# Performance work log

Measured on AMD Instinct MI355X. Metric: run time of the kernel, lower is better.

The kernel has to match this reference:

```python
import jax, jax.numpy as jnp
import numpy as np

N, E, G = 20000, 320000, 64
IN, HID, HEADS, EDGE_D, ACT = 128, 256, 4, 5, 8
NEG_SLOPE = 0.2


def setup_inputs() -> dict:
    key = jax.random.key(0)
    ks = jax.random.split(key, 24)
    g = lambda i, shape, scale=0.05: jax.random.normal(ks[i], shape, dtype=jnp.float32) * scale
    inp = {
        "x": jax.random.normal(ks[0], (N, IN), dtype=jnp.float32),
        "edge_index": jax.random.randint(ks[1], (2, E), 0, N, dtype=jnp.int64),
        "batch": jnp.sort(jax.random.randint(ks[2], (N,), 0, G, dtype=jnp.int64)),
        "edge_attr": jax.random.normal(ks[3], (E, EDGE_D), dtype=jnp.float32),
        # GATv2 layer 1: in->64 per head, 4 heads, concat -> 256
        "W1l": g(4, (IN, HID)), "W1r": g(5, (IN, HID)), "W1e": g(6, (EDGE_D, HID)),
        "att1": g(7, (HEADS, HID // HEADS)), "b1": jnp.zeros((HID,), jnp.float32),
        # GATv2 layer 2: 256->256, 1 head
        "W2l": g(8, (HID, HID)), "W2r": g(9, (HID, HID)), "W2e": g(10, (EDGE_D, HID)),
        "att2": g(11, (1, HID)), "b2": jnp.zeros((HID,), jnp.float32),
        # heads
        "Wp": g(12, (HID, ACT)), "bp": jnp.zeros((ACT,), jnp.float32),
        "Wv": g(13, (HID, 1)), "bv": jnp.zeros((1,), jnp.float32),
    }
    return inp


def gatv2_conv(x, src, dst, edge_attr, Wl, Wr, We, att, bias, heads, concat):
    # PyG GATv2Conv (share_weights=False, add_self_loops=False):
    #   x_l = lin_l(x) (source msg), x_r = lin_r(x) (target), e = lin_edge(edge_attr)
    #   score = att . leaky_relu(x_l[src] + x_r[dst] + e); segment-softmax over dst
    #   out[i] = sum_j alpha_ij * x_l[j]
    n = x.shape[0]
    c = Wl.shape[1] // heads
    xl = (x @ Wl).reshape(n, heads, c)
    xr = (x @ Wr).reshape(n, heads, c)
    e = (edge_attr @ We).reshape(-1, heads, c)
    m = jax.nn.leaky_relu(xl[src] + xr[dst] + e, NEG_SLOPE)      # [E, H, C]
    logit = jnp.einsum("ehc,hc->eh", m, att)                      # [E, H]
    lmax = jax.ops.segment_max(logit, dst, num_segments=n)        # [N, H]
    unnorm = jnp.exp(logit - lmax[dst])
    denom = jax.ops.segment_sum(unnorm, dst, num_segments=n)
    alpha = unnorm / (denom[dst] + 1e-16)                         # [E, H]
    out = jax.ops.segment_sum(alpha[:, :, None] * xl[src], dst, num_segments=n)  # [N,H,C]
    out = out.reshape(n, heads * c) if concat else out.mean(axis=1)
    return out + bias


def reference(x, edge_index, batch, edge_attr,
              W1l, W1r, W1e, att1, b1,
              W2l, W2r, W2e, att2, b2,
              Wp, bp, Wv, bv):
    src, dst = edge_index[0], edge_index[1]
    h = gatv2_conv(x, src, dst, edge_attr, W1l, W1r, W1e, att1, b1, HEADS, True)
    h = jax.nn.relu(h)  # dropout p=0.0 -> identity
    h = gatv2_conv(h, src, dst, edge_attr, W2l, W2r, W2e, att2, b2, 1, False)
    h = jax.nn.relu(h)
    # global mean pool over graphs
    sums = jax.ops.segment_sum(h, batch, num_segments=G)
    cnt = jax.ops.segment_sum(jnp.ones((h.shape[0],), h.dtype), batch, num_segments=G)
    g = sums / jnp.maximum(cnt, 1.0)[:, None]
    logits = g @ Wp + bp                 # [G, ACT]
    value = (g @ Wv + bv)[:, 0]          # [G]
    # deterministic outputs (sampling excluded): concat logits and value
    return jnp.concatenate([logits, value[:, None]], axis=-1)  # [G, ACT+1]
```

## Files before the change

### kernel.cpp

```cpp
#include <hip/hip_runtime.h>
#include <math.h>

#define NN 20000
#define NE 320000
#define NG 64
#define IND 128
#define HIDD 256
#define NH 4
#define ED 5
#define NACT 8
#define NEG 0.2f
#define MAXDEG 64

__global__ __launch_bounds__(256) void gemm64(const float* __restrict__ A,
    const float* __restrict__ B, float* __restrict__ C, int M, int K, int Ncol)
{
    const int BK = 32;
    __shared__ float As[32][68];
    __shared__ float Bs[32][64];
    int bm = blockIdx.x * 64, bn = blockIdx.y * 64;
    int tid = threadIdx.x;
    int tx = tid & 15, ty = tid >> 4;
    float acc[4][4] = {};
    for (int k0 = 0; k0 < K; k0 += BK) {
        for (int idx = tid; idx < 64 * BK; idx += 256) {
            int r = idx >> 5, c = idx & 31;
            int gr = bm + r;
            As[c][r] = (gr < M) ? A[(size_t)gr * K + k0 + c] : 0.f;
        }
        for (int idx = tid; idx < BK * 64; idx += 256) {
            int r = idx >> 6, c = idx & 63;
            Bs[r][c] = B[(size_t)(k0 + r) * Ncol + bn + c];
        }
        __syncthreads();
        #pragma unroll
        for (int k = 0; k < BK; ++k) {
            float4 a4 = *(const float4*)&As[k][ty * 4];
            float4 b4 = *(const float4*)&Bs[k][tx * 4];
            float a[4] = {a4.x, a4.y, a4.z, a4.w};
            float b[4] = {b4.x, b4.y, b4.z, b4.w};
            #pragma unroll
            for (int i = 0; i < 4; ++i)
                #pragma unroll
                for (int j = 0; j < 4; ++j)
                    acc[i][j] = fmaf(a[i], b[j], acc[i][j]);
        }
        __syncthreads();
    }
    #pragma unroll
    for (int i = 0; i < 4; ++i) {
        int r = bm + ty * 4 + i;
        if (r < M) {
            float4 v = {acc[i][0], acc[i][1], acc[i][2], acc[i][3]};
            *(float4*)&C[(size_t)r * Ncol + bn + tx * 4] = v;
        }
    }
}

__global__ __launch_bounds__(256) void build_slots(const int* __restrict__ dst,
    int* __restrict__ deg, int* __restrict__ slots)
{
    int e = blockIdx.x * 256 + threadIdx.x;
    if (e >= NE) return;
    int d = dst[e];
    int pos = atomicAdd(&deg[d], 1);
    if (pos < MAXDEG) slots[d * MAXDEG + pos] = e;
}

template <int HEADS_T>
__global__ __launch_bounds__(256) void fused_agg(
    const int* __restrict__ deg, const int* __restrict__ slots,
    const int* __restrict__ src, const float* __restrict__ eattr,
    const float* __restrict__ xl, const float* __restrict__ xr,
    const float* __restrict__ We, const float* __restrict__ attw,
    const float* __restrict__ bias, float* __restrict__ out)
{
    __shared__ float sWe[ED * HIDD];
    __shared__ float sAtt[HIDD];
    for (int i = threadIdx.x; i < ED * HIDD; i += 256) sWe[i] = We[i];
    for (int i = threadIdx.x; i < HIDD; i += 256) sAtt[i] = attw[i];
    __syncthreads();

    int wave = threadIdx.x >> 6, lane = threadIdx.x & 63;
    int n = blockIdx.x * 4 + wave;
    int dg = min(deg[n], MAXDEG);
    int c0 = lane * 4;

    float attr_[4], wer[ED][4];
    #pragma unroll
    for (int j = 0; j < 4; ++j) attr_[j] = sAtt[c0 + j];
    #pragma unroll
    for (int k = 0; k < ED; ++k)
        #pragma unroll
        for (int j = 0; j < 4; ++j) wer[k][j] = sWe[k * HIDD + c0 + j];

    float4 xr4 = *(const float4*)(xr + (size_t)n * HIDD + c0);
    float xra[4] = {xr4.x, xr4.y, xr4.z, xr4.w};

    float denom = 0.f;
    float acc[4] = {0.f, 0.f, 0.f, 0.f};

    const int* slotrow = slots + (size_t)n * MAXDEG;
    for (int i = 0; i < dg; ++i) {
        int e = slotrow[i];
        int s = src[e];
        float4 xl4 = *(const float4*)(xl + (size_t)s * HIDD + c0);
        float xla[4] = {xl4.x, xl4.y, xl4.z, xl4.w};
        float ea[ED];
        #pragma unroll
        for (int k = 0; k < ED; ++k) ea[k] = eattr[(size_t)e * ED + k];
        float partial = 0.f;
        #pragma unroll
        for (int j = 0; j < 4; ++j) {
            float ev = 0.f;
            #pragma unroll
            for (int k = 0; k < ED; ++k) ev = fmaf(ea[k], wer[k][j], ev);
            float m = xla[j] + xra[j] + ev;
            m = m > 0.f ? m : NEG * m;
            partial = fmaf(m, attr_[j], partial);
        }
        if (HEADS_T == 4) {
            #pragma unroll
            for (int off = 1; off < 16; off <<= 1)
                partial += __shfl_xor(partial, off, 64);
        } else {
            #pragma unroll
            for (int off = 1; off < 64; off <<= 1)
                partial += __shfl_xor(partial, off, 64);
        }
        float ex = expf(partial);
        denom += ex;
        #pragma unroll
        for (int j = 0; j < 4; ++j) acc[j] = fmaf(ex, xla[j], acc[j]);
    }
    float inv = 1.f / (denom + 1e-16f);
    float4 o;
    o.x = fmaxf(acc[0] * inv + bias[c0 + 0], 0.f);
    o.y = fmaxf(acc[1] * inv + bias[c0 + 1], 0.f);
    o.z = fmaxf(acc[2] * inv + bias[c0 + 2], 0.f);
    o.w = fmaxf(acc[3] * inv + bias[c0 + 3], 0.f);
    *(float4*)(out + (size_t)n * HIDD + c0) = o;
}

#define POOL_CHUNK 128
__global__ __launch_bounds__(256) void pool_kernel(
    const float* __restrict__ h, const int* __restrict__ batch,
    float* __restrict__ pool, float* __restrict__ cnt)
{
    int c = threadIdx.x;
    int start = blockIdx.x * POOL_CHUNK;
    int end = min(start + POOL_CHUNK, NN);
    if (start >= NN) return;
    float acc = 0.f;
    int cur = batch[start];
    int localCount = 0;
    for (int n = start; n < end; ++n) {
        int g = batch[n];
        if (g != cur) {
            atomicAdd(&pool[cur * HIDD + c], acc);
            if (c == 0) atomicAdd(&cnt[cur], (float)localCount);
            acc = 0.f; localCount = 0; cur = g;
        }
        acc += h[(size_t)n * HIDD + c];
        ++localCount;
    }
    atomicAdd(&pool[cur * HIDD + c], acc);
    if (c == 0) atomicAdd(&cnt[cur], (float)localCount);
}

__global__ __launch_bounds__(256) void head_kernel(
    const float* __restrict__ pool, const float* __restrict__ cnt,
    const float* __restrict__ Wp, const float* __restrict__ bp,
    const float* __restrict__ Wv, const float* __restrict__ bv,
    float* __restrict__ out)
{
    int g = blockIdx.x;
    int c = threadIdx.x;
    float gv = pool[g * HIDD + c] / fmaxf(cnt[g], 1.0f);
    __shared__ float red[256];
    for (int j = 0; j < NACT + 1; ++j) {
        float w = (j < NACT) ? Wp[c * NACT + j] : Wv[c];
        red[c] = gv * w;
        __syncthreads();
        for (int sl = 128; sl > 0; sl >>= 1) {
            if (c < sl) red[c] += red[c + sl];
            __syncthreads();
        }
        if (c == 0) out[g * (NACT + 1) + j] = red[0] + ((j < NACT) ? bp[j] : bv[0]);
        __syncthreads();
    }
}

extern "C" void kernel_launch(void* const* d_in, const int* in_sizes, int n_in,
                              void* d_out, int out_size, void* d_ws, size_t ws_size,
                              hipStream_t stream)
{
    const float* x    = (const float*)d_in[0];
    const int*   ei   = (const int*)d_in[1];
    const int*   batch= (const int*)d_in[2];
    const float* ea   = (const float*)d_in[3];
    const float* W1l  = (const float*)d_in[4];
    const float* W1r  = (const float*)d_in[5];
    const float* W1e  = (const float*)d_in[6];
    const float* att1 = (const float*)d_in[7];
    const float* b1   = (const float*)d_in[8];
    const float* W2l  = (const float*)d_in[9];
    const float* W2r  = (const float*)d_in[10];
    const float* W2e  = (const float*)d_in[11];
    const float* att2 = (const float*)d_in[12];
    const float* b2   = (const float*)d_in[13];
    const float* Wp   = (const float*)d_in[14];
    const float* bp   = (const float*)d_in[15];
    const float* Wv   = (const float*)d_in[16];
    const float* bv   = (const float*)d_in[17];
    const int* src = ei;
    const int* dst = ei + NE;
    float* out = (float*)d_out;

    float* ws = (float*)d_ws;
    size_t off = 0;
    float* A     = ws + off; off += (size_t)NN * HIDD;
    float* B     = ws + off; off += (size_t)NN * HIDD;
    float* C     = ws + off; off += (size_t)NN * HIDD;
    float* D     = ws + off; off += (size_t)NN * HIDD;
    float* pool  = ws + off; off += (size_t)NG * HIDD;
    float* cnt   = ws + off; off += NG;
    int*   deg   = (int*)(ws + off); off += NN;
    int*   slots = (int*)(ws + off); off += (size_t)NN * MAXDEG;

    hipMemsetAsync(pool, 0, (size_t)(NG * HIDD + NG + NN) * sizeof(float), stream);

    build_slots<<<(NE + 255) / 256, 256, 0, stream>>>(dst, deg, slots);

    dim3 ggrid((NN + 63) / 64, HIDD / 64);
    gemm64<<<ggrid, 256, 0, stream>>>(x, W1l, A, NN, IND, HIDD);
    gemm64<<<ggrid, 256, 0, stream>>>(x, W1r, B, NN, IND, HIDD);
    fused_agg<4><<<NN / 4, 256, 0, stream>>>(deg, slots, src, ea, A, B, W1e, att1, b1, C);

    gemm64<<<ggrid, 256, 0, stream>>>(C, W2l, A, NN, HIDD, HIDD);
    gemm64<<<ggrid, 256, 0, stream>>>(C, W2r, B, NN, HIDD, HIDD);
    fused_agg<1><<<NN / 4, 256, 0, stream>>>(deg, slots, src, ea, A, B, W2e, att2, b2, D);

    pool_kernel<<<(NN + POOL_CHUNK - 1) / POOL_CHUNK, 256, 0, stream>>>(D, batch, pool, cnt);
    head_kernel<<<NG, 256, 0, stream>>>(pool, cnt, Wp, bp, Wv, bv, out);
}
```

Before: 485.0 us.

## Enlarge GEMM tiles, batch l/r GEMMs, and prefetch edge data per lane in aggregation

The GEMM now uses 128x64 tiles with 8x4 outputs per thread and handles both left and right weight matrices in one launch via blockIdx.z, halving the launches and raising reuse per thread. The aggregation kernel preloads each neighbour's slot, source index and edge attributes into one lane each, then broadcasts them with shuffles instead of reloading them serially. It also processes two edges per iteration so their gathers and reductions overlap. Register pressure goes up in both kernels, and the As padding of 129 may cause LDS bank conflicts or misaligned float4 reads.

```diff
diff --git a/kernel.cpp b/kernel.cpp
--- a/kernel.cpp
+++ b/kernel.cpp
@@ -12,35 +12,43 @@
 #define NEG 0.2f
 #define MAXDEG 64
 
-__global__ __launch_bounds__(256) void gemm64(const float* __restrict__ A,
-    const float* __restrict__ B, float* __restrict__ C, int M, int K, int Ncol)
-{
-    const int BK = 32;
-    __shared__ float As[32][68];
+__global__ __launch_bounds__(256) void gemm128x64(
+    const float* __restrict__ A, const float* __restrict__ Bl,
+    const float* __restrict__ Br, float* __restrict__ Cl, float* __restrict__ Cr,
+    int M, int K, int Ncol)
+{
+    const float* B = blockIdx.z ? Br : Bl;
+    float*       C = blockIdx.z ? Cr : Cl;
+    __shared__ float As[32][129];
     __shared__ float Bs[32][64];
-    int bm = blockIdx.x * 64, bn = blockIdx.y * 64;
+    int bm = blockIdx.x * 128, bn = blockIdx.y * 64;
     int tid = threadIdx.x;
     int tx = tid & 15, ty = tid >> 4;
-    float acc[4][4] = {};
-    for (int k0 = 0; k0 < K; k0 += BK) {
-        for (int idx = tid; idx < 64 * BK; idx += 256) {
+    float acc[8][4] = {};
+    for (int k0 = 0; k0 < K; k0 += 32) {
+        #pragma unroll
+        for (int t = 0; t < 16; ++t) {
+            int idx = tid + t * 256;
             int r = idx >> 5, c = idx & 31;
             int gr = bm + r;
             As[c][r] = (gr < M) ? A[(size_t)gr * K + k0 + c] : 0.f;
         }
-        for (int idx = tid; idx < BK * 64; idx += 256) {
+        #pragma unroll
+        for (int t = 0; t < 8; ++t) {
+            int idx = tid + t * 256;
             int r = idx >> 6, c = idx & 63;
             Bs[r][c] = B[(size_t)(k0 + r) * Ncol + bn + c];
         }
         __syncthreads();
         #pragma unroll
-        for (int k = 0; k < BK; ++k) {
-            float4 a4 = *(const float4*)&As[k][ty * 4];
-            float4 b4 = *(const float4*)&Bs[k][tx * 4];
-            float a[4] = {a4.x, a4.y, a4.z, a4.w};
-            float b[4] = {b4.x, b4.y, b4.z, b4.w};
-            #pragma unroll
-            for (int i = 0; i < 4; ++i)
+        for (int k = 0; k < 32; ++k) {
+            float4 a0 = *(const float4*)&As[k][ty * 8];
+            float4 a1 = *(const float4*)&As[k][ty * 8 + 4];
+            float4 b0 = *(const float4*)&Bs[k][tx * 4];
+            float a[8] = {a0.x, a0.y, a0.z, a0.w, a1.x, a1.y, a1.z, a1.w};
+            float b[4] = {b0.x, b0.y, b0.z, b0.w};
+            #pragma unroll
+            for (int i = 0; i < 8; ++i)
                 #pragma unroll
                 for (int j = 0; j < 4; ++j)
                     acc[i][j] = fmaf(a[i], b[j], acc[i][j]);
@@ -48,8 +56,8 @@
         __syncthreads();
     }
     #pragma unroll
-    for (int i = 0; i < 4; ++i) {
-        int r = bm + ty * 4 + i;
+    for (int i = 0; i < 8; ++i) {
+        int r = bm + ty * 8 + i;
         if (r < M) {
             float4 v = {acc[i][0], acc[i][1], acc[i][2], acc[i][3]};
             *(float4*)&C[(size_t)r * Ncol + bn + tx * 4] = v;
@@ -97,42 +105,100 @@
     float4 xr4 = *(const float4*)(xr + (size_t)n * HIDD + c0);
     float xra[4] = {xr4.x, xr4.y, xr4.z, xr4.w};
 
+    int s_l = 0;
+    float ea_l[ED] = {0.f, 0.f, 0.f, 0.f, 0.f};
+    if (lane < dg) {
+        int e_l = slots[(size_t)n * MAXDEG + lane];
+        s_l = src[e_l];
+        #pragma unroll
+        for (int k = 0; k < ED; ++k) ea_l[k] = eattr[(size_t)e_l * ED + k];
+    }
+
     float denom = 0.f;
     float acc[4] = {0.f, 0.f, 0.f, 0.f};
 
-    const int* slotrow = slots + (size_t)n * MAXDEG;
-    for (int i = 0; i < dg; ++i) {
-        int e = slotrow[i];
-        int s = src[e];
-        float4 xl4 = *(const float4*)(xl + (size_t)s * HIDD + c0);
-        float xla[4] = {xl4.x, xl4.y, xl4.z, xl4.w};
-        float ea[ED];
-        #pragma unroll
-        for (int k = 0; k < ED; ++k) ea[k] = eattr[(size_t)e * ED + k];
-        float partial = 0.f;
+    int i = 0;
+    for (; i + 2 <= dg; i += 2) {
+        int sA = __shfl(s_l, i, 64);
+        int sB = __shfl(s_l, i + 1, 64);
+        float eaA[ED], eaB[ED];
+        #pragma unroll
+        for (int k = 0; k < ED; ++k) {
+            eaA[k] = __shfl(ea_l[k], i, 64);
+            eaB[k] = __shfl(ea_l[k], i + 1, 64);
+        }
+        float4 xA4 = *(const float4*)(xl + (size_t)sA * HIDD + c0);
+        float4 xB4 = *(const float4*)(xl + (size_t)sB * HIDD + c0);
+        float xlA[4] = {xA4.x, xA4.y, xA4.z, xA4.w};
+        float xlB[4] = {xB4.x, xB4.y, xB4.z, xB4.w};
+        float pA = 0.f, pB = 0.f;
         #pragma unroll
         for (int j = 0; j < 4; ++j) {
-            float ev = 0.f;
-            #pragma unroll
-            for (int k = 0; k < ED; ++k) ev = fmaf(ea[k], wer[k][j], ev);
-            float m = xla[j] + xra[j] + ev;
-            m = m > 0.f ? m : NEG * m;
-            partial = fmaf(m, attr_[j], partial);
+            float evA = 0.f, evB = 0.f;
+            #pragma unroll
+            for (int k = 0; k < ED; ++k) {
+                evA = fmaf(eaA[k], wer[k][j], evA);
+                evB = fmaf(eaB[k], wer[k][j], evB);
+            }
+            float mA = xlA[j] + xra[j] + evA;
+            float mB = xlB[j] + xra[j] + evB;
+            mA = mA > 0.f ? mA : NEG * mA;
+            mB = mB > 0.f ? mB : NEG * mB;
+            pA = fmaf(mA, attr_[j], pA);
+            pB = fmaf(mB, attr_[j], pB);
         }
         if (HEADS_T == 4) {
             #pragma unroll
-            for (int off = 1; off < 16; off <<= 1)
-                partial += __shfl_xor(partial, off, 64);
+            for (int off = 1; off < 16; off <<= 1) {
+                pA += __shfl_xor(pA, off, 64);
+                pB += __shfl_xor(pB, off, 64);
+            }
         } else {
             #pragma unroll
-            for (int off = 1; off < 64; off <<= 1)
-                partial += __shfl_xor(partial, off, 64);
-        }
-        float ex = expf(partial);
-        denom += ex;
-        #pragma unroll
-        for (int j = 0; j < 4; ++j) acc[j] = fmaf(ex, xla[j], acc[j]);
-    }
+            for (int off = 1; off < 64; off <<= 1) {
+                pA += __shfl_xor(pA, off, 64);
+                pB += __shfl_xor(pB, off, 64);
+            }
+        }
+        float exA = expf(pA);
+        float exB = expf(pB);
+        denom += exA;
+        denom += exB;
+        #pragma unroll
+        for (int j = 0; j < 4; ++j) acc[j] = fmaf(exA, xlA[j], acc[j]);
+        #pragma unroll
+        for (int j = 0; j < 4; ++j) acc[j] = fmaf(exB, xlB[j], acc[j]);
+    }
+    if (i < dg) {
+        int sA = __shfl(s_l, i, 64);
+        float eaA[ED];
+        #pragma unroll
+        for (int k = 0; k < ED; ++k) eaA[k] = __shfl(ea_l[k], i, 64);
+        float4 xA4 = *(const float4*)(xl + (size_t)sA * HIDD + c0);
+        float xlA[4] = {xA4.x, xA4.y, xA4.z, xA4.w};
+        float pA = 0.f;
+        #pragma unroll
+        for (int j = 0; j < 4; ++j) {
+            float evA = 0.f;
+            #pragma unroll
+            for (int k = 0; k < ED; ++k) evA = fmaf(eaA[k], wer[k][j], evA);
+            float mA = xlA[j] + xra[j] + evA;
+            mA = mA > 0.f ? mA : NEG * mA;
+            pA = fmaf(mA, attr_[j], pA);
+        }
+        if (HEADS_T == 4) {
+            #pragma unroll
+            for (int off = 1; off < 16; off <<= 1) pA += __shfl_xor(pA, off, 64);
+        } else {
+            #pragma unroll
+            for (int off = 1; off < 64; off <<= 1) pA += __shfl_xor(pA, off, 64);
+        }
+        float exA = expf(pA);
+        denom += exA;
+        #pragma unroll
+        for (int j = 0; j < 4; ++j) acc[j] = fmaf(exA, xlA[j], acc[j]);
+    }
+
     float inv = 1.f / (denom + 1e-16f);
     float4 o;
     o.x = fmaxf(acc[0] * inv + bias[c0 + 0], 0.f);
@@ -232,13 +298,11 @@
 
     build_slots<<<(NE + 255) / 256, 256, 0, stream>>>(dst, deg, slots);
 
-    dim3 ggrid((NN + 63) / 64, HIDD / 64);
-    gemm64<<<ggrid, 256, 0, stream>>>(x, W1l, A, NN, IND, HIDD);
-    gemm64<<<ggrid, 256, 0, stream>>>(x, W1r, B, NN, IND, HIDD);
+    dim3 g1((NN + 127) / 128, HIDD / 64, 2);
+    gemm128x64<<<g1, 256, 0, stream>>>(x, W1l, W1r, A, B, NN, IND, HIDD);
     fused_agg<4><<<NN / 4, 256, 0, stream>>>(deg, slots, src, ea, A, B, W1e, att1, b1, C);
 
-    gemm64<<<ggrid, 256, 0, stream>>>(C, W2l, A, NN, HIDD, HIDD);
-    gemm64<<<ggrid, 256, 0, stream>>>(C, W2r, B, NN, HIDD, HIDD);
+    gemm128x64<<<g1, 256, 0, stream>>>(C, W2l, W2r, A, B, NN, HIDD, HIDD);
     fused_agg<1><<<NN / 4, 256, 0, stream>>>(deg, slots, src, ea, A, B, W2e, att2, b2, D);
 
     pool_kernel<<<(NN + POOL_CHUNK - 1) / POOL_CHUNK, 256, 0, stream>>>(D, batch, pool, cnt);
```

Result: slower. 666.1 us (+37.4%).
